# Kernel optimization log

Measured on AMD Instinct MI355X. Metric: run time of the kernel, lower is better.

Reference implementation:

```python
import jax, jax.numpy as jnp
import numpy as np

H, W = 256, 256
L = 1024
R = 4
B = 64
EPS = 1e-4
FF = (H + W) * R * 4


def setup_inputs() -> dict:
    key = jax.random.key(0)
    ks = jax.random.split(key, 8)
    x = jax.random.normal(ks[0], (B, L), dtype=jnp.float32)
    # Linear weights (torch Linear: out = x @ W.T), kaiming-uniform-ish init
    lim = 1.0 / np.sqrt(L)
    W_t = jax.random.uniform(ks[1], (FF, L), minval=-lim, maxval=lim, dtype=jnp.float32)
    W_g = jax.random.uniform(ks[2], (FF, L), minval=-lim, maxval=lim, dtype=jnp.float32)
    # weights_static: [2, H, W, 2]
    k_lim = np.sqrt(6.0 / (H * W))
    ws0 = jax.random.uniform(ks[3], (1, H, W, 2), minval=-k_lim, maxval=k_lim, dtype=jnp.float32)
    ws1_re = jax.random.uniform(ks[4], (1, H, W, 1), minval=EPS - 1.0, maxval=1.0 - EPS, dtype=jnp.float32)
    ws1_im = jax.random.uniform(ks[5], (1, H, W, 1), minval=-EPS, maxval=EPS, dtype=jnp.float32)
    weights_static = jnp.concatenate([ws0, jnp.concatenate([ws1_re, ws1_im], axis=-1)], axis=0)
    x_lim = np.sqrt(6.0 / (H + W))
    weights_mod = jax.random.uniform(ks[6], (4, H, W), minval=-x_lim, maxval=x_lim, dtype=jnp.float32)
    c_lim = 1.0 / np.sqrt(R)
    kc1, kc2 = jax.random.split(ks[7])
    conv_w = jax.random.uniform(kc1, (R, R), minval=-c_lim, maxval=c_lim, dtype=jnp.float32)  # [out_ch, in_ch] for 1x1 conv
    conv_b = jax.random.uniform(kc2, (R,), minval=-c_lim, maxval=c_lim, dtype=jnp.float32)
    return {"x": x, "W_t": W_t, "W_g": W_g, "weights_static": weights_static,
            "weights_mod": weights_mod, "conv_w": conv_w, "conv_b": conv_b}


def reference(x, W_t, W_g, weights_static, weights_mod, conv_w, conv_b):
    b = x.shape[0]
    xt = x @ W_t.T                                  # [B, FF]
    xg = x @ W_g.T
    xg = xg * jax.nn.sigmoid(xg)                    # SiLU-style gate
    mod = xt * xg
    mod = mod.reshape(b, 4, -1)
    mod = mod / jnp.sqrt(jnp.mean(jnp.abs(mod), axis=-1, keepdims=True) + EPS)
    mod = mod.reshape(b, 4, R, H + W)
    a_part = mod[..., :H]                           # [B,4,R,H]
    b_part = mod[..., H:]                           # [B,4,R,W]
    outer = jnp.einsum('bkri,bkrj->bkrij', a_part, b_part)  # [B,4,R,H,W]
    # 1x1 conv (R->R) followed by sum over output channels collapses to a
    # single contraction with column-summed weights + summed bias (same math).
    w_eff = conv_w.sum(axis=0)                      # [R]
    b_eff = conv_b.sum()
    mod = jnp.einsum('bkrij,r->bkij', outer, w_eff) + b_eff  # [B,4,H,W]
    mod = weights_mod[None] * mod
    A0 = weights_static[0]                          # [H,W,2]
    A1 = weights_static[1]                          # [H,W,2]
    Bc = jnp.moveaxis(mod[:, 0:2], 1, -1)           # [B,H,W,2]
    re = A1[..., 0] * Bc[..., 0] - A1[..., 1] * Bc[..., 1]
    im = A1[..., 0] * Bc[..., 1] - A1[..., 1] * Bc[..., 0]
    mag = jnp.sqrt(re * re + im * im + EPS)         # [B,H,W]
    mag = jnp.sqrt(jnp.mean(mag, axis=(-1, -2)) + EPS)  # [B]
    inv = 1.0 / mag[:, None, None]
    mw_re = A0[..., 0] + re * inv                   # [B,H,W]
    mw_im = A0[..., 1] + im * inv
    proj = jnp.moveaxis(mod[:, 2:4], 1, -1)         # [B,H,W,2]
    den = jnp.sqrt(proj[..., 0] ** 2 + proj[..., 1] ** 2 + EPS)
    theta_cos = proj[..., 0] / den
    theta_sin = proj[..., 1] / den
    return mw_re * theta_cos + mw_im * theta_sin    # [B,H,W]
```

## Files before the change

### kernel.cpp

```cpp
#include <hip/hip_runtime.h>

typedef __bf16 bf16x8 __attribute__((ext_vector_type(8)));
typedef float floatx4 __attribute__((ext_vector_type(4)));

__device__ inline void cvt8_hl(const float* __restrict__ p, bf16x8& h, bf16x8& l){
  float4 v0 = *reinterpret_cast<const float4*>(p);
  float4 v1 = *reinterpret_cast<const float4*>(p + 4);
  float v[8] = {v0.x, v0.y, v0.z, v0.w, v1.x, v1.y, v1.z, v1.w};
  #pragma unroll
  for (int i = 0; i < 8; ++i) {
    __bf16 hi = (__bf16)v[i];
    h[i] = hi;
    l[i] = (__bf16)(v[i] - (float)hi);
  }
}

__global__ __launch_bounds__(256) void k1_gemm(
    const float* __restrict__ x,
    const float* __restrict__ Wt,
    const float* __restrict__ Wg,
    float* __restrict__ mod)
{
  __shared__ float red[3][32][64];
  const int tid  = threadIdx.x;
  const int wave = tid >> 6, lane = tid & 63;
  const int quad = lane >> 4, r16 = lane & 15;
  const int ff = blockIdx.x * 16 + r16;
  const int kb = wave * 256 + quad * 8;

  floatx4 accT[4], accG[4];
  #pragma unroll
  for (int m = 0; m < 4; ++m) { accT[m] = (floatx4)0.0f; accG[m] = (floatx4)0.0f; }

  const float* wt = Wt + ff * 1024 + kb;
  const float* wg = Wg + ff * 1024 + kb;
  const float* xp = x  + r16 * 1024 + kb;

  #pragma unroll
  for (int it = 0; it < 8; ++it) {
    const int ko = it * 32;
    bf16x8 bth, btl, bgh, bgl;
    cvt8_hl(wt + ko, bth, btl);
    cvt8_hl(wg + ko, bgh, bgl);
    #pragma unroll
    for (int mt = 0; mt < 4; ++mt) {
      bf16x8 ah, al;
      cvt8_hl(xp + mt * 16384 + ko, ah, al);
      accT[mt] = __builtin_amdgcn_mfma_f32_16x16x32_bf16(ah, bth, accT[mt], 0, 0, 0);
      accT[mt] = __builtin_amdgcn_mfma_f32_16x16x32_bf16(ah, btl, accT[mt], 0, 0, 0);
      accT[mt] = __builtin_amdgcn_mfma_f32_16x16x32_bf16(al, bth, accT[mt], 0, 0, 0);
      accG[mt] = __builtin_amdgcn_mfma_f32_16x16x32_bf16(ah, bgh, accG[mt], 0, 0, 0);
      accG[mt] = __builtin_amdgcn_mfma_f32_16x16x32_bf16(ah, bgl, accG[mt], 0, 0, 0);
      accG[mt] = __builtin_amdgcn_mfma_f32_16x16x32_bf16(al, bgh, accG[mt], 0, 0, 0);
    }
  }

  if (wave != 0) {
    #pragma unroll
    for (int mt = 0; mt < 4; ++mt)
      #pragma unroll
      for (int r = 0; r < 4; ++r) {
        red[wave - 1][mt * 4 + r][lane]      = accT[mt][r];
        red[wave - 1][16 + mt * 4 + r][lane] = accG[mt][r];
      }
  }
  __syncthreads();
  if (wave == 0) {
    #pragma unroll
    for (int mt = 0; mt < 4; ++mt) {
      #pragma unroll
      for (int r = 0; r < 4; ++r) {
        float t = accT[mt][r] + red[0][mt * 4 + r][lane]
                              + red[1][mt * 4 + r][lane]
                              + red[2][mt * 4 + r][lane];
        float g = accG[mt][r] + red[0][16 + mt * 4 + r][lane]
                              + red[1][16 + mt * 4 + r][lane]
                              + red[2][16 + mt * 4 + r][lane];
        float sig = 1.0f / (1.0f + __expf(-g));
        int b = mt * 16 + quad * 4 + r;
        mod[b * 8192 + ff] = t * g * sig;
      }
    }
  }
}

__global__ __launch_bounds__(256) void k1b_scale(const float* __restrict__ mod,
                                                 float* __restrict__ s)
{
  const int row = blockIdx.x;
  const int tid = threadIdx.x;
  const float* p = mod + row * 2048;
  float sum = 0.0f;
  #pragma unroll
  for (int q = 0; q < 8; ++q) sum += fabsf(p[q * 256 + tid]);
  #pragma unroll
  for (int o = 1; o < 64; o <<= 1) sum += __shfl_xor(sum, o, 64);
  __shared__ float ls[4];
  if ((tid & 63) == 0) ls[tid >> 6] = sum;
  __syncthreads();
  if (tid == 0) {
    float t = ls[0] + ls[1] + ls[2] + ls[3];
    s[row] = rsqrtf(t * (1.0f / 2048.0f) + 1e-4f);
  }
}

__global__ __launch_bounds__(256) void k2_mag(
    const float* __restrict__ mod, const float* __restrict__ s,
    const float* __restrict__ wstat,
    const float* __restrict__ wmod,
    const float* __restrict__ cw,
    const float* __restrict__ cb,
    float* __restrict__ partial)
{
  const int b = blockIdx.x, jc = blockIdx.y, isplit = blockIdx.z;
  const int tid = threadIdx.x;
  __shared__ __align__(16) float a_l[64 * 8];

  float weff[4]; float beff = 0.0f;
  #pragma unroll
  for (int r = 0; r < 4; ++r) {
    weff[r] = cw[r] + cw[4 + r] + cw[8 + r] + cw[12 + r];
    beff += cb[r];
  }
  const float s0 = s[b * 4 + 0], s1 = s[b * 4 + 1];
  const float* mb = mod + b * 8192;

  #pragma unroll
  for (int q = 0; q < 2; ++q) {
    int e = q * 256 + tid;
    int il = e & 63, p = e >> 6;
    int k = p >> 2, r = p & 3;
    a_l[il * 8 + p] = mb[k * 2048 + r * 512 + isplit * 64 + il] * ((k ? s1 : s0) * weff[r]);
  }
  const int j = jc * 32 + (tid & 31);
  float bp[8];
  #pragma unroll
  for (int p = 0; p < 8; ++p) {
    int k = p >> 2, r = p & 3;
    bp[p] = mb[k * 2048 + r * 512 + 256 + j] * (k ? s1 : s0);
  }
  __syncthreads();

  const int ioff = tid >> 5;
  float acc = 0.0f;
  #pragma unroll
  for (int it = 0; it < 8; ++it) {
    const int il = it * 8 + ioff;
    const int i = isplit * 64 + il;
    const float4 av0 = *reinterpret_cast<const float4*>(&a_l[il * 8]);
    const float4 av1 = *reinterpret_cast<const float4*>(&a_l[il * 8 + 4]);
    float d0 = av0.x * bp[0] + av0.y * bp[1] + av0.z * bp[2] + av0.w * bp[3];
    float d1 = av1.x * bp[4] + av1.y * bp[5] + av1.z * bp[6] + av1.w * bp[7];
    const int ij = i * 256 + j;
    float m0 = wmod[ij] * (d0 + beff);
    float m1 = wmod[65536 + ij] * (d1 + beff);
    float2 a1 = *reinterpret_cast<const float2*>(wstat + 131072 + ij * 2);
    float re = a1.x * m0 - a1.y * m1;
    float im = a1.x * m1 - a1.y * m0;
    acc += sqrtf(re * re + im * im + 1e-4f);
  }
  #pragma unroll
  for (int o = 1; o < 64; o <<= 1) acc += __shfl_xor(acc, o, 64);
  __shared__ float wsum[4];
  if ((tid & 63) == 0) wsum[tid >> 6] = acc;
  __syncthreads();
  if (tid == 0) atomicAdd(&partial[b * 8 + jc], wsum[0] + wsum[1] + wsum[2] + wsum[3]);
}

__global__ __launch_bounds__(256) void k4_out(
    const float* __restrict__ mod, const float* __restrict__ s,
    const float* __restrict__ wstat,
    const float* __restrict__ wmod,
    const float* __restrict__ cw,
    const float* __restrict__ cb,
    const float* __restrict__ partial,
    float* __restrict__ out)
{
  const int b = blockIdx.x, ibase = blockIdx.y * 8;
  const int tid = threadIdx.x;
  __shared__ __align__(16) float a_l[8 * 16];

  float weff[4]; float beff = 0.0f;
  #pragma unroll
  for (int r = 0; r < 4; ++r) {
    weff[r] = cw[r] + cw[4 + r] + cw[8 + r] + cw[12 + r];
    beff += cb[r];
  }
  float sk[4];
  #pragma unroll
  for (int k = 0; k < 4; ++k) sk[k] = s[b * 4 + k];
  const float* mb = mod + b * 8192;

  float tot = 0.0f;
  #pragma unroll
  for (int t = 0; t < 8; ++t) tot += partial[b * 8 + t];
  const float inv = rsqrtf(tot * (1.0f / 65536.0f) + 1e-4f);

  if (tid < 128) {
    int il = tid & 7, kr = tid >> 3;
    int k = kr >> 2, r = kr & 3;
    a_l[il * 16 + kr] = mb[k * 2048 + r * 512 + ibase + il] * (sk[k] * weff[r]);
  }
  const int j = (tid & 127) * 2;
  const int ioff = tid >> 7;
  float bp0[16], bp1[16];
  #pragma unroll
  for (int kr = 0; kr < 16; ++kr) {
    int k = kr >> 2, r = kr & 3;
    float2 v = *reinterpret_cast<const float2*>(mb + k * 2048 + r * 512 + 256 + j);
    bp0[kr] = v.x * sk[k]; bp1[kr] = v.y * sk[k];
  }
  __syncthreads();

  #pragma unroll
  for (int it = 0; it < 4; ++it) {
    const int il = it * 2 + ioff;
    const int i = ibase + il;
    const float4 a0 = *reinterpret_cast<const float4*>(&a_l[il * 16]);
    const float4 a1 = *reinterpret_cast<const float4*>(&a_l[il * 16 + 4]);
    const float4 a2 = *reinterpret_cast<const float4*>(&a_l[il * 16 + 8]);
    const float4 a3 = *reinterpret_cast<const float4*>(&a_l[il * 16 + 12]);
    const int ij = i * 256 + j;
    const float2 wm0 = *reinterpret_cast<const float2*>(wmod + ij);
    const float2 wm1 = *reinterpret_cast<const float2*>(wmod + 65536 + ij);
    const float2 wm2 = *reinterpret_cast<const float2*>(wmod + 131072 + ij);
    const float2 wm3 = *reinterpret_cast<const float2*>(wmod + 196608 + ij);
    const float4 A0v = *reinterpret_cast<const float4*>(wstat + ij * 2);
    const float4 A1v = *reinterpret_cast<const float4*>(wstat + 131072 + ij * 2);
    float outv[2];
    #pragma unroll
    for (int e = 0; e < 2; ++e) {
      const float* bp = e ? bp1 : bp0;
      float d0 = a0.x * bp[0] + a0.y * bp[1] + a0.z * bp[2] + a0.w * bp[3];
      float d1 = a1.x * bp[4] + a1.y * bp[5] + a1.z * bp[6] + a1.w * bp[7];
      float d2 = a2.x * bp[8] + a2.y * bp[9] + a2.z * bp[10] + a2.w * bp[11];
      float d3 = a3.x * bp[12] + a3.y * bp[13] + a3.z * bp[14] + a3.w * bp[15];
      float m0 = (e ? wm0.y : wm0.x) * (d0 + beff);
      float m1 = (e ? wm1.y : wm1.x) * (d1 + beff);
      float m2 = (e ? wm2.y : wm2.x) * (d2 + beff);
      float m3 = (e ? wm3.y : wm3.x) * (d3 + beff);
      float A0r = e ? A0v.z : A0v.x;
      float A0i = e ? A0v.w : A0v.y;
      float A1r = e ? A1v.z : A1v.x;
      float A1i = e ? A1v.w : A1v.y;
      float re = A1r * m0 - A1i * m1;
      float im = A1r * m1 - A1i * m0;
      float mwre = A0r + re * inv;
      float mwim = A0i + im * inv;
      float rd = rsqrtf(m2 * m2 + m3 * m3 + 1e-4f);
      outv[e] = (mwre * m2 + mwim * m3) * rd;
    }
    *reinterpret_cast<float2*>(out + b * 65536 + ij) = make_float2(outv[0], outv[1]);
  }
}

extern "C" void kernel_launch(void* const* d_in, const int* in_sizes, int n_in,
                              void* d_out, int out_size, void* d_ws, size_t ws_size,
                              hipStream_t stream) {
  const float* x     = (const float*)d_in[0];
  const float* Wt    = (const float*)d_in[1];
  const float* Wg    = (const float*)d_in[2];
  const float* wstat = (const float*)d_in[3];
  const float* wmod  = (const float*)d_in[4];
  const float* cw    = (const float*)d_in[5];
  const float* cb    = (const float*)d_in[6];

  float* mod     = (float*)d_ws;
  float* sbuf    = mod + 524288;
  float* partial = sbuf + 256;

  hipMemsetAsync(partial, 0, 512 * sizeof(float), stream);
  k1_gemm  <<<512, 256, 0, stream>>>(x, Wt, Wg, mod);
  k1b_scale<<<256, 256, 0, stream>>>(mod, sbuf);
  k2_mag   <<<dim3(64, 8, 4), 256, 0, stream>>>(mod, sbuf, wstat, wmod, cw, cb, partial);
  k4_out   <<<dim3(64, 32), 256, 0, stream>>>(mod, sbuf, wstat, wmod, cw, cb, partial,
                                              (float*)d_out);
}
```

Baseline: 154.7 us.

## Tile k2/k4 over spatial (i,j) blocks and loop over batch for weight reuse

Both the magnitude and output kernels are re-gridded so that each block owns an 8x32 spatial tile and iterates over all 64 batch items in groups of 8. The per-pixel static weights (wmod, wstat) are then loaded once per block instead of once per batch item, which cuts repeated global traffic on those arrays. The rank factors are staged through shared memory each group, and the per-batch partial sums are collected in shared memory before one atomic per batch. The trade-offs are far fewer blocks (256 instead of 2048), a serial loop with two barriers per group, scalar rather than float2 output stores, and per-wave shuffle reductions plus shared atomics inside the loop.

```diff
diff --git a/kernel.cpp b/kernel.cpp
--- a/kernel.cpp
+++ b/kernel.cpp
@@ -112,9 +112,16 @@
     const float* __restrict__ cb,
     float* __restrict__ partial)
 {
-  const int b = blockIdx.x, jc = blockIdx.y, isplit = blockIdx.z;
+  const int ibase = blockIdx.x * 8, jbase = blockIdx.y * 32;
   const int tid = threadIdx.x;
-  __shared__ __align__(16) float a_l[64 * 8];
+  const int il = tid >> 5, jl = tid & 31;
+  const int i = ibase + il, j = jbase + jl;
+  const int ij = i * 256 + j;
+
+  __shared__ float a_l[8][8][8];
+  __shared__ float bp_l[8][32][12];
+  __shared__ float sk_l[256];
+  __shared__ float bsum[64];
 
   float weff[4]; float beff = 0.0f;
   #pragma unroll
@@ -122,49 +129,51 @@
     weff[r] = cw[r] + cw[4 + r] + cw[8 + r] + cw[12 + r];
     beff += cb[r];
   }
-  const float s0 = s[b * 4 + 0], s1 = s[b * 4 + 1];
-  const float* mb = mod + b * 8192;
-
-  #pragma unroll
-  for (int q = 0; q < 2; ++q) {
-    int e = q * 256 + tid;
-    int il = e & 63, p = e >> 6;
-    int k = p >> 2, r = p & 3;
-    a_l[il * 8 + p] = mb[k * 2048 + r * 512 + isplit * 64 + il] * ((k ? s1 : s0) * weff[r]);
-  }
-  const int j = jc * 32 + (tid & 31);
-  float bp[8];
-  #pragma unroll
-  for (int p = 0; p < 8; ++p) {
-    int k = p >> 2, r = p & 3;
-    bp[p] = mb[k * 2048 + r * 512 + 256 + j] * (k ? s1 : s0);
-  }
-  __syncthreads();
-
-  const int ioff = tid >> 5;
-  float acc = 0.0f;
-  #pragma unroll
-  for (int it = 0; it < 8; ++it) {
-    const int il = it * 8 + ioff;
-    const int i = isplit * 64 + il;
-    const float4 av0 = *reinterpret_cast<const float4*>(&a_l[il * 8]);
-    const float4 av1 = *reinterpret_cast<const float4*>(&a_l[il * 8 + 4]);
-    float d0 = av0.x * bp[0] + av0.y * bp[1] + av0.z * bp[2] + av0.w * bp[3];
-    float d1 = av1.x * bp[4] + av1.y * bp[5] + av1.z * bp[6] + av1.w * bp[7];
-    const int ij = i * 256 + j;
-    float m0 = wmod[ij] * (d0 + beff);
-    float m1 = wmod[65536 + ij] * (d1 + beff);
-    float2 a1 = *reinterpret_cast<const float2*>(wstat + 131072 + ij * 2);
-    float re = a1.x * m0 - a1.y * m1;
-    float im = a1.x * m1 - a1.y * m0;
-    acc += sqrtf(re * re + im * im + 1e-4f);
-  }
-  #pragma unroll
-  for (int o = 1; o < 64; o <<= 1) acc += __shfl_xor(acc, o, 64);
-  __shared__ float wsum[4];
-  if ((tid & 63) == 0) wsum[tid >> 6] = acc;
-  __syncthreads();
-  if (tid == 0) atomicAdd(&partial[b * 8 + jc], wsum[0] + wsum[1] + wsum[2] + wsum[3]);
+  sk_l[tid] = s[tid];
+  if (tid < 64) bsum[tid] = 0.0f;
+  const float wm0 = wmod[ij];
+  const float wm1 = wmod[65536 + ij];
+  const float2 A1 = *reinterpret_cast<const float2*>(wstat + 131072 + ij * 2);
+  __syncthreads();
+
+  for (int g = 0; g < 8; ++g) {
+    const int b0 = g * 8;
+    #pragma unroll
+    for (int q = 0; q < 2; ++q) {
+      int ee = q * 256 + tid;
+      int bb = ee >> 6, kr = (ee >> 3) & 7, i2 = ee & 7;
+      int b = b0 + bb, k = kr >> 2, r = kr & 3;
+      a_l[bb][i2][kr] = mod[b * 8192 + k * 2048 + r * 512 + ibase + i2]
+                        * (sk_l[b * 4 + k] * weff[r]);
+    }
+    {
+      int kr = tid >> 5, k = kr >> 2, r = kr & 3;
+      #pragma unroll
+      for (int bb = 0; bb < 8; ++bb) {
+        int b = b0 + bb;
+        bp_l[bb][jl][kr] = mod[b * 8192 + k * 2048 + r * 512 + 256 + j]
+                           * sk_l[b * 4 + k];
+      }
+    }
+    __syncthreads();
+    #pragma unroll
+    for (int bb = 0; bb < 8; ++bb) {
+      const float* ap  = a_l[bb][il];
+      const float* bpp = bp_l[bb][jl];
+      float d0 = ap[0]*bpp[0] + ap[1]*bpp[1] + ap[2]*bpp[2] + ap[3]*bpp[3];
+      float d1 = ap[4]*bpp[4] + ap[5]*bpp[5] + ap[6]*bpp[6] + ap[7]*bpp[7];
+      float m0 = wm0 * (d0 + beff);
+      float m1 = wm1 * (d1 + beff);
+      float re = A1.x * m0 - A1.y * m1;
+      float im = A1.x * m1 - A1.y * m0;
+      float mg = sqrtf(re * re + im * im + 1e-4f);
+      #pragma unroll
+      for (int o = 1; o < 64; o <<= 1) mg += __shfl_xor(mg, o, 64);
+      if ((tid & 63) == 0) atomicAdd(&bsum[b0 + bb], mg);
+    }
+    __syncthreads();
+  }
+  if (tid < 64) atomicAdd(&partial[tid], bsum[tid]);
 }
 
 __global__ __launch_bounds__(256) void k4_out(
@@ -176,9 +185,16 @@
     const float* __restrict__ partial,
     float* __restrict__ out)
 {
-  const int b = blockIdx.x, ibase = blockIdx.y * 8;
+  const int ibase = blockIdx.x * 8, jbase = blockIdx.y * 32;
   const int tid = threadIdx.x;
-  __shared__ __align__(16) float a_l[8 * 16];
+  const int il = tid >> 5, jl = tid & 31;
+  const int i = ibase + il, j = jbase + jl;
+  const int ij = i * 256 + j;
+
+  __shared__ __align__(16) float a_l[8][8][16];
+  __shared__ __align__(16) float bp_l[8][32][20];
+  __shared__ float sk_l[256];
+  __shared__ float inv_l[64];
 
   float weff[4]; float beff = 0.0f;
   #pragma unroll
@@ -186,71 +202,68 @@
     weff[r] = cw[r] + cw[4 + r] + cw[8 + r] + cw[12 + r];
     beff += cb[r];
   }
-  float sk[4];
-  #pragma unroll
-  for (int k = 0; k < 4; ++k) sk[k] = s[b * 4 + k];
-  const float* mb = mod + b * 8192;
-
-  float tot = 0.0f;
-  #pragma unroll
-  for (int t = 0; t < 8; ++t) tot += partial[b * 8 + t];
-  const float inv = rsqrtf(tot * (1.0f / 65536.0f) + 1e-4f);
-
-  if (tid < 128) {
-    int il = tid & 7, kr = tid >> 3;
-    int k = kr >> 2, r = kr & 3;
-    a_l[il * 16 + kr] = mb[k * 2048 + r * 512 + ibase + il] * (sk[k] * weff[r]);
-  }
-  const int j = (tid & 127) * 2;
-  const int ioff = tid >> 7;
-  float bp0[16], bp1[16];
-  #pragma unroll
-  for (int kr = 0; kr < 16; ++kr) {
-    int k = kr >> 2, r = kr & 3;
-    float2 v = *reinterpret_cast<const float2*>(mb + k * 2048 + r * 512 + 256 + j);
-    bp0[kr] = v.x * sk[k]; bp1[kr] = v.y * sk[k];
-  }
-  __syncthreads();
-
-  #pragma unroll
-  for (int it = 0; it < 4; ++it) {
-    const int il = it * 2 + ioff;
-    const int i = ibase + il;
-    const float4 a0 = *reinterpret_cast<const float4*>(&a_l[il * 16]);
-    const float4 a1 = *reinterpret_cast<const float4*>(&a_l[il * 16 + 4]);
-    const float4 a2 = *reinterpret_cast<const float4*>(&a_l[il * 16 + 8]);
-    const float4 a3 = *reinterpret_cast<const float4*>(&a_l[il * 16 + 12]);
-    const int ij = i * 256 + j;
-    const float2 wm0 = *reinterpret_cast<const float2*>(wmod + ij);
-    const float2 wm1 = *reinterpret_cast<const float2*>(wmod + 65536 + ij);
-    const float2 wm2 = *reinterpret_cast<const float2*>(wmod + 131072 + ij);
-    const float2 wm3 = *reinterpret_cast<const float2*>(wmod + 196608 + ij);
-    const float4 A0v = *reinterpret_cast<const float4*>(wstat + ij * 2);
-    const float4 A1v = *reinterpret_cast<const float4*>(wstat + 131072 + ij * 2);
-    float outv[2];
-    #pragma unroll
-    for (int e = 0; e < 2; ++e) {
-      const float* bp = e ? bp1 : bp0;
-      float d0 = a0.x * bp[0] + a0.y * bp[1] + a0.z * bp[2] + a0.w * bp[3];
-      float d1 = a1.x * bp[4] + a1.y * bp[5] + a1.z * bp[6] + a1.w * bp[7];
-      float d2 = a2.x * bp[8] + a2.y * bp[9] + a2.z * bp[10] + a2.w * bp[11];
-      float d3 = a3.x * bp[12] + a3.y * bp[13] + a3.z * bp[14] + a3.w * bp[15];
-      float m0 = (e ? wm0.y : wm0.x) * (d0 + beff);
-      float m1 = (e ? wm1.y : wm1.x) * (d1 + beff);
-      float m2 = (e ? wm2.y : wm2.x) * (d2 + beff);
-      float m3 = (e ? wm3.y : wm3.x) * (d3 + beff);
-      float A0r = e ? A0v.z : A0v.x;
-      float A0i = e ? A0v.w : A0v.y;
-      float A1r = e ? A1v.z : A1v.x;
-      float A1i = e ? A1v.w : A1v.y;
-      float re = A1r * m0 - A1i * m1;
-      float im = A1r * m1 - A1i * m0;
-      float mwre = A0r + re * inv;
-      float mwim = A0i + im * inv;
+  sk_l[tid] = s[tid];
+  if (tid < 64) inv_l[tid] = rsqrtf(partial[tid] * (1.0f / 65536.0f) + 1e-4f);
+  const float wm0 = wmod[ij];
+  const float wm1 = wmod[65536  + ij];
+  const float wm2 = wmod[131072 + ij];
+  const float wm3 = wmod[196608 + ij];
+  const float2 A0 = *reinterpret_cast<const float2*>(wstat + ij * 2);
+  const float2 A1 = *reinterpret_cast<const float2*>(wstat + 131072 + ij * 2);
+  __syncthreads();
+
+  for (int g = 0; g < 8; ++g) {
+    const int b0 = g * 8;
+    #pragma unroll
+    for (int q = 0; q < 4; ++q) {
+      int ee = q * 256 + tid;
+      int bb = ee >> 7, kr = (ee >> 3) & 15, i2 = ee & 7;
+      int b = b0 + bb, k = kr >> 2, r = kr & 3;
+      a_l[bb][i2][kr] = mod[b * 8192 + k * 2048 + r * 512 + ibase + i2]
+                        * (sk_l[b * 4 + k] * weff[r]);
+    }
+    {
+      int kr0 = tid >> 5;
+      #pragma unroll
+      for (int bb = 0; bb < 8; ++bb) {
+        int b = b0 + bb;
+        #pragma unroll
+        for (int h = 0; h < 2; ++h) {
+          int kr = kr0 + h * 8, k = kr >> 2, r = kr & 3;
+          bp_l[bb][jl][kr] = mod[b * 8192 + k * 2048 + r * 512 + 256 + j]
+                             * sk_l[b * 4 + k];
+        }
+      }
+    }
+    __syncthreads();
+    #pragma unroll
+    for (int bb = 0; bb < 8; ++bb) {
+      const int b = b0 + bb;
+      const float4 a0 = *reinterpret_cast<const float4*>(&a_l[bb][il][0]);
+      const float4 a1 = *reinterpret_cast<const float4*>(&a_l[bb][il][4]);
+      const float4 a2 = *reinterpret_cast<const float4*>(&a_l[bb][il][8]);
+      const float4 a3 = *reinterpret_cast<const float4*>(&a_l[bb][il][12]);
+      const float4 b0v = *reinterpret_cast<const float4*>(&bp_l[bb][jl][0]);
+      const float4 b1v = *reinterpret_cast<const float4*>(&bp_l[bb][jl][4]);
+      const float4 b2v = *reinterpret_cast<const float4*>(&bp_l[bb][jl][8]);
+      const float4 b3v = *reinterpret_cast<const float4*>(&bp_l[bb][jl][12]);
+      float d0 = a0.x*b0v.x + a0.y*b0v.y + a0.z*b0v.z + a0.w*b0v.w;
+      float d1 = a1.x*b1v.x + a1.y*b1v.y + a1.z*b1v.z + a1.w*b1v.w;
+      float d2 = a2.x*b2v.x + a2.y*b2v.y + a2.z*b2v.z + a2.w*b2v.w;
+      float d3 = a3.x*b3v.x + a3.y*b3v.y + a3.z*b3v.z + a3.w*b3v.w;
+      float m0 = wm0 * (d0 + beff);
+      float m1 = wm1 * (d1 + beff);
+      float m2 = wm2 * (d2 + beff);
+      float m3 = wm3 * (d3 + beff);
+      float re = A1.x * m0 - A1.y * m1;
+      float im = A1.x * m1 - A1.y * m0;
+      float inv = inv_l[b];
+      float mwre = A0.x + re * inv;
+      float mwim = A0.y + im * inv;
       float rd = rsqrtf(m2 * m2 + m3 * m3 + 1e-4f);
-      outv[e] = (mwre * m2 + mwim * m3) * rd;
-    }
-    *reinterpret_cast<float2*>(out + b * 65536 + ij) = make_float2(outv[0], outv[1]);
+      out[b * 65536 + ij] = (mwre * m2 + mwim * m3) * rd;
+    }
+    __syncthreads();
   }
 }
 
@@ -269,10 +282,10 @@
   float* sbuf    = mod + 524288;
   float* partial = sbuf + 256;
 
-  hipMemsetAsync(partial, 0, 512 * sizeof(float), stream);
+  hipMemsetAsync(partial, 0, 64 * sizeof(float), stream);
   k1_gemm  <<<512, 256, 0, stream>>>(x, Wt, Wg, mod);
   k1b_scale<<<256, 256, 0, stream>>>(mod, sbuf);
-  k2_mag   <<<dim3(64, 8, 4), 256, 0, stream>>>(mod, sbuf, wstat, wmod, cw, cb, partial);
-  k4_out   <<<dim3(64, 32), 256, 0, stream>>>(mod, sbuf, wstat, wmod, cw, cb, partial,
-                                              (float*)d_out);
-}
+  k2_mag   <<<dim3(32, 8), 256, 0, stream>>>(mod, sbuf, wstat, wmod, cw, cb, partial);
+  k4_out   <<<dim3(32, 8), 256, 0, stream>>>(mod, sbuf, wstat, wmod, cw, cb, partial,
+                                             (float*)d_out);
+}
```

Result: slower. 213.3 us (+37.9%).
